# Optimization experiments

Hardware: AMD Instinct MI355X
Metric: run time of the kernel (lower is better)

Reference implementation:

```python
import jax, jax.numpy as jnp
import numpy as np

FACTOR = 3.0  # maxval of the per-image std uniform draw


def setup_inputs() -> dict:
    key = jax.random.key(0)
    k1, k2 = jax.random.split(key)
    x = jax.random.uniform(k1, (64, 512, 512, 3), dtype=jnp.float32)
    stds = jax.random.uniform(k2, (64,), dtype=jnp.float32)  # uniform [0,1), scaled by FACTOR in reference
    return {"x": x, "stds": stds}


def reference(x, stds):
    # Faithful port of AddingGaussianBlur. Note the original has ys = tf.cast(xs, ...)
    # (a bug), so the kernel depends only on the column coordinate; we reproduce it.
    B, H, W, C = x.shape
    std = stds * FACTOR  # per-image std ~ Uniform(0, factor), shape [B]
    xs_row = jnp.arange(-1, 2, dtype=jnp.float32)          # [-1, 0, 1]
    xs = jnp.broadcast_to(xs_row[None, :], (3, 3))          # meshgrid xs (rows repeat)
    s = std[:, None, None]                                  # [B,1,1]
    # k = exp(-(xs^2 + ys^2)/(2 std^2)) / (2 pi std^2) with ys == xs
    k = jnp.exp(-(xs**2 + xs**2) / (2.0 * s**2)) / (2.0 * np.pi * s**2)  # [B,3,3]
    k = k / jnp.sum(k, axis=(1, 2), keepdims=True)
    # SAME zero-padded 3x3 cross-correlation, same kernel for all 3 channels,
    # per-sample kernel: expressed as weighted sum of 9 shifted views (fully batched).
    xpad = jnp.pad(x, ((0, 0), (1, 1), (1, 1), (0, 0)))
    out = jnp.zeros_like(x)
    for di in range(3):
        for dj in range(3):
            out = out + k[:, di, dj][:, None, None, None] * xpad[:, di:di + H, dj:dj + W, :]
    return out
```

## Files before the change

### kernel.cpp

```cpp
#include <hip/hip_runtime.h>
#include <math.h>


constexpr int Wd   = 512;
constexpr int Hd   = 512;
constexpr int Cd   = 3;
constexpr int ROWF = Wd * Cd;
constexpr int TPB  = ROWF / 4;

__global__ __launch_bounds__(TPB) void gauss_row_kernel(
    const float* __restrict__ x,
    const float* __restrict__ stds,
    float* __restrict__ out)
{
    __shared__ float4 cs[TPB + 2];

    const int t  = threadIdx.x;
    const int bi = blockIdx.x;
    const int i  = bi & (Hd - 1);
    const int b  = bi >> 9;

    const float s  = stds[b] * 3.0f;
    const float e  = expf(-1.0f / (s * s));
    const float w1 = 1.0f / (3.0f * (1.0f + 2.0f * e));
    const float w0 = e * w1;

    const float* row = x + (size_t)bi * ROWF + (size_t)t * 4;

    float4 m = *(const float4*)(row);
    if (i > 0) {
        float4 a = *(const float4*)(row - ROWF);
        m.x += a.x; m.y += a.y; m.z += a.z; m.w += a.w;
    }
    if (i < Hd - 1) {
        float4 a = *(const float4*)(row + ROWF);
        m.x += a.x; m.y += a.y; m.z += a.z; m.w += a.w;
    }

    if (t == 0) {
        cs[0]       = make_float4(0.f, 0.f, 0.f, 0.f);
        cs[TPB + 1] = make_float4(0.f, 0.f, 0.f, 0.f);
    }
    cs[t + 1] = m;
    __syncthreads();

    const float4 p = cs[t];
    const float4 n = cs[t + 2];

    float4 o;
    o.x = w1 * m.x + w0 * (p.y + m.w);
    o.y = w1 * m.y + w0 * (p.z + n.x);
    o.z = w1 * m.z + w0 * (p.w + n.y);
    o.w = w1 * m.w + w0 * (m.x + n.z);

    ((float4*)(out + (size_t)bi * ROWF))[t] = o;
}

extern "C" void kernel_launch(void* const* d_in, const int* in_sizes, int n_in,
                              void* d_out, int out_size, void* d_ws, size_t ws_size,
                              hipStream_t stream) {
    const float* x    = (const float*)d_in[0];
    const float* stds = (const float*)d_in[1];
    float* out        = (float*)d_out;

    const int nblocks = 64 * Hd;
    gauss_row_kernel<<<nblocks, TPB, 0, stream>>>(x, stds, out);
}
```

Baseline: 336.0 us.

## Process 32-row strips per wavefront with register row reuse and shuffle halos

Replaces the one-block-per-row kernel with wavefronts that each walk a 32-row strip of one 256-float4 column segment. Rows are kept in registers as a rolling window, so each input row is loaded about once per strip instead of three times. Horizontal neighbours now come from wave shuffles plus edge-lane halo loads, which removes the shared memory and __syncthreads. The cost is halo reloads at segment and strip boundaries, extra branching for the edge lanes, and fewer, longer-running waves.

Measured after the change: 345.8 us. +2.9%, slower.

```diff
diff --git a/kernel.cpp b/kernel.cpp
--- a/kernel.cpp
+++ b/kernel.cpp
@@ -6,54 +6,85 @@
 constexpr int Hd   = 512;
 constexpr int Cd   = 3;
 constexpr int ROWF = Wd * Cd;
-constexpr int TPB  = ROWF / 4;
+constexpr int SEGS = ROWF / (64*4);
+constexpr int RS   = 32;
+constexpr int NSTR = Hd / RS;
+constexpr int TPB  = 256;
 
-__global__ __launch_bounds__(TPB) void gauss_row_kernel(
+__device__ __forceinline__ float4 f4zero() { return make_float4(0.f,0.f,0.f,0.f); }
+__device__ __forceinline__ float4 f4add3(float4 a, float4 b, float4 c) {
+    return make_float4(a.x+b.x+c.x, a.y+b.y+c.y, a.z+b.z+c.z, a.w+b.w+c.w);
+}
+
+__global__ __launch_bounds__(TPB) void gauss_strip_kernel(
     const float* __restrict__ x,
     const float* __restrict__ stds,
     float* __restrict__ out)
 {
-    __shared__ float4 cs[TPB + 2];
-
-    const int t  = threadIdx.x;
-    const int bi = blockIdx.x;
-    const int i  = bi & (Hd - 1);
-    const int b  = bi >> 9;
+    const int lane = threadIdx.x & 63;
+    const int w    = blockIdx.x * (TPB/64) + (threadIdx.x >> 6);
+    const int strip = w & (NSTR - 1);
+    const int seg   = (w >> 4) % SEGS;
+    const int b     = w / (NSTR * SEGS);
 
     const float s  = stds[b] * 3.0f;
     const float e  = expf(-1.0f / (s * s));
     const float w1 = 1.0f / (3.0f * (1.0f + 2.0f * e));
     const float w0 = e * w1;
 
-    const float* row = x + (size_t)bi * ROWF + (size_t)t * 4;
+    const int f4 = seg * 64 + lane;
+    const size_t imgoff = (size_t)b * Hd * ROWF + (size_t)f4 * 4;
+    const float* cb  = x   + imgoff;
+    float*       cbo = out + imgoff;
 
-    float4 m = *(const float4*)(row);
-    if (i > 0) {
-        float4 a = *(const float4*)(row - ROWF);
-        m.x += a.x; m.y += a.y; m.z += a.z; m.w += a.w;
+    const bool haloL = (lane == 0)  && (seg > 0);
+    const bool haloR = (lane == 63) && (seg < SEGS - 1);
+    const bool halo  = haloL || haloR;
+    const int  hoff  = haloL ? -4 : 4;
+
+    const int r0 = strip * RS;
+
+    float4 rprev = f4zero(), rcur, hprev = f4zero(), hcur = f4zero();
+
+    if (r0 > 0) {
+        rprev = *(const float4*)(cb + (size_t)(r0-1) * ROWF);
+        if (halo) hprev = *(const float4*)(cb + (size_t)(r0-1) * ROWF + hoff);
     }
-    if (i < Hd - 1) {
-        float4 a = *(const float4*)(row + ROWF);
-        m.x += a.x; m.y += a.y; m.z += a.z; m.w += a.w;
+    rcur = *(const float4*)(cb + (size_t)r0 * ROWF);
+    if (halo) hcur = *(const float4*)(cb + (size_t)r0 * ROWF + hoff);
+
+    #pragma unroll 4
+    for (int k = 0; k < RS; ++k) {
+        const int r = r0 + k;
+        float4 rnext = f4zero(), hnext = f4zero();
+        if (r + 1 < Hd) {
+            rnext = *(const float4*)(cb + (size_t)(r+1) * ROWF);
+            if (halo) hnext = *(const float4*)(cb + (size_t)(r+1) * ROWF + hoff);
+        }
+
+        const float4 m  = f4add3(rprev, rcur, rnext);
+        const float4 mh = f4add3(hprev, hcur, hnext);
+
+        float py = __shfl_up(m.y, 1);
+        float pz = __shfl_up(m.z, 1);
+        float pw = __shfl_up(m.w, 1);
+        float nx = __shfl_down(m.x, 1);
+        float ny = __shfl_down(m.y, 1);
+        float nz = __shfl_down(m.z, 1);
+        if (lane == 0)  { py = mh.y; pz = mh.z; pw = mh.w; }
+        if (lane == 63) { nx = mh.x; ny = mh.y; nz = mh.z; }
+
+        float4 o;
+        o.x = w1 * m.x + w0 * (py  + m.w);
+        o.y = w1 * m.y + w0 * (pz  + nx);
+        o.z = w1 * m.z + w0 * (pw  + ny);
+        o.w = w1 * m.w + w0 * (m.x + nz);
+
+        *(float4*)(cbo + (size_t)r * ROWF) = o;
+
+        rprev = rcur; rcur = rnext;
+        hprev = hcur; hcur = hnext;
     }
-
-    if (t == 0) {
-        cs[0]       = make_float4(0.f, 0.f, 0.f, 0.f);
-        cs[TPB + 1] = make_float4(0.f, 0.f, 0.f, 0.f);
-    }
-    cs[t + 1] = m;
-    __syncthreads();
-
-    const float4 p = cs[t];
-    const float4 n = cs[t + 2];
-
-    float4 o;
-    o.x = w1 * m.x + w0 * (p.y + m.w);
-    o.y = w1 * m.y + w0 * (p.z + n.x);
-    o.z = w1 * m.z + w0 * (p.w + n.y);
-    o.w = w1 * m.w + w0 * (m.x + n.z);
-
-    ((float4*)(out + (size_t)bi * ROWF))[t] = o;
 }
 
 extern "C" void kernel_launch(void* const* d_in, const int* in_sizes, int n_in,
@@ -63,6 +94,7 @@
     const float* stds = (const float*)d_in[1];
     float* out        = (float*)d_out;
 
-    const int nblocks = 64 * Hd;
-    gauss_row_kernel<<<nblocks, TPB, 0, stream>>>(x, stds, out);
+    const int nwaves  = 64 * SEGS * NSTR;
+    const int nblocks = nwaves / (TPB / 64);
+    gauss_strip_kernel<<<nblocks, TPB, 0, stream>>>(x, stds, out);
 }
```
